# Kernel tuning notes

Measured on AMD Instinct MI355X. Metric: run time of the kernel, lower is better.

## Reference

```python
import jax, jax.numpy as jnp
import numpy as np
import math

N_HEADS = 8

def _head_dirs():
    # 8 trigrams = corners of {-1,+1}^3, L2-normalized -> each row / sqrt(3)
    t = np.array([[ (i >> 2 & 1) * 2 - 1, (i >> 1 & 1) * 2 - 1, (i & 1) * 2 - 1]
                  for i in range(8)], dtype=np.float32)
    return jnp.asarray(t / np.sqrt(3.0, dtype=np.float32))

def setup_inputs() -> dict:
    key = jax.random.key(0)
    k1, k2, k3, k4 = jax.random.split(key, 4)
    B, T, C = 2, 2048, 1024
    x = jax.random.normal(k1, (B, T, C), dtype=jnp.float32)
    w_qkv = jax.random.normal(k2, (C, 3 * C), dtype=jnp.float32) * (1.0 / math.sqrt(C))
    w_out = jax.random.normal(k3, (C, C), dtype=jnp.float32) * (1.0 / math.sqrt(C))
    head_scales = jax.random.normal(k4, (N_HEADS,), dtype=jnp.float32) * 0.1
    return {"x": x, "w_qkv": w_qkv, "w_out": w_out, "head_scales": head_scales}

def reference(x, w_qkv, w_out, head_scales):
    B, T, C = x.shape
    H = N_HEADS
    hd = C // H
    scale = 1.0 / math.sqrt(hd)
    dirs = _head_dirs()  # [H,3], fixed buffer

    qkv = (x @ w_qkv).reshape(B, T, 3, H, hd)
    q = jnp.transpose(qkv[:, :, 0], (0, 2, 1, 3))  # [B,H,T,hd]
    k = jnp.transpose(qkv[:, :, 1], (0, 2, 1, 3))
    v = jnp.transpose(qkv[:, :, 2], (0, 2, 1, 3))

    scores = jnp.einsum('bhqd,bhkd->bhqk', q, k) * scale  # [B,H,T,T]
    causal = jnp.tril(jnp.ones((T, T), dtype=bool))
    scores = jnp.where(causal[None, None], scores, -jnp.inf)

    # rank-1 geometric (trigram) bias on first 3 dims of q,k
    q_proj = jnp.einsum('bhtd,hd->bht', q[..., :3], dirs)  # [B,H,T]
    k_proj = jnp.einsum('bhtd,hd->bht', k[..., :3], dirs)
    geo = q_proj[..., :, None] * k_proj[..., None, :]       # [B,H,T,T]
    scores = scores + head_scales[None, :, None, None] * geo

    attn = jax.nn.softmax(scores, axis=-1)
    out = jnp.einsum('bhqk,bhkd->bqhd', attn, v).reshape(B, T, C)
    return out @ w_out
```

## Files before the change

### kernel.cpp

```cpp
#include <hip/hip_runtime.h>
#include <hip/hip_bf16.h>
#include <cstdint>
#include <cstddef>


namespace {
constexpr int kB = 2, kT = 2048, kC = 1024, kHD = 128;
constexpr int kM = kB * kT;
constexpr int kN3 = 3 * kC;
constexpr float kScale = 0.08838834764831845f;
constexpr float kInvS3 = 0.57735026918962576f;
constexpr float kL2E  = 1.4426950408889634f;
}

typedef __bf16 bf16x8 __attribute__((ext_vector_type(8)));
typedef float f32x4 __attribute__((ext_vector_type(4)));
typedef unsigned short u16x8 __attribute__((ext_vector_type(8)));
typedef unsigned short u16x4 __attribute__((ext_vector_type(4)));
typedef unsigned int u32x4 __attribute__((ext_vector_type(4)));

__device__ __forceinline__ unsigned short f2b(float f) {
  return __builtin_bit_cast(unsigned short, (__bf16)f);
}
__device__ __forceinline__ float b2f(unsigned short u) {
  return (float)__builtin_bit_cast(__bf16, u);
}
__device__ __forceinline__ void gll16(const void* g, void* lds) {
  __builtin_amdgcn_global_load_lds(
      (const __attribute__((address_space(1))) unsigned int*)g,
      (__attribute__((address_space(3))) unsigned int*)lds, 16, 0, 0);
}
__device__ __forceinline__ bf16x8 ldsv(const unsigned short* p) {
  return __builtin_bit_cast(bf16x8, *(const u16x8*)p);
}
__device__ __forceinline__ uint2 tr16(const unsigned short* p) {
  uint2 r;
  unsigned off = (unsigned)(uintptr_t)(const __attribute__((address_space(3))) unsigned short*)p;
  asm volatile("ds_read_b64_tr_b16 %0, %1" : "=v"(r) : "v"(off));
  return r;
}

__global__ void k_cvt(const float* __restrict__ in, unsigned short* __restrict__ out, int n4) {
  int i = blockIdx.x * 256 + threadIdx.x;
  if (i >= n4) return;
  float4 v = ((const float4*)in)[i];
  u16x4 o = { f2b(v.x), f2b(v.y), f2b(v.z), f2b(v.w) };
  ((u16x4*)out)[i] = o;
}

__global__ void k_tc(const float* __restrict__ in, unsigned short* __restrict__ out,
                     int R, int Cin) {
  __shared__ float tile[64][65];
  const int t = threadIdx.x;
  const int r0 = blockIdx.y * 64, c0 = blockIdx.x * 64;
  const int tr = t >> 4, tc4 = (t & 15) * 4;
#pragma unroll
  for (int rr = 0; rr < 4; ++rr) {
    int r = tr + rr * 16;
    float4 v = *(const float4*)&in[(size_t)(r0 + r) * Cin + c0 + tc4];
    tile[r][tc4 + 0] = v.x; tile[r][tc4 + 1] = v.y;
    tile[r][tc4 + 2] = v.z; tile[r][tc4 + 3] = v.w;
  }
  __syncthreads();
#pragma unroll
  for (int rr = 0; rr < 4; ++rr) {
    int c = tr + rr * 16;
    u16x4 o = { f2b(tile[tc4 + 0][c]), f2b(tile[tc4 + 1][c]),
                f2b(tile[tc4 + 2][c]), f2b(tile[tc4 + 3][c]) };
    *(u16x4*)&out[(size_t)(c0 + c) * R + r0 + tc4] = o;
  }
}

__global__ __launch_bounds__(256, 2) void k_gemm(
    const unsigned short* __restrict__ A,
    const unsigned short* __restrict__ Bt,
    unsigned short* __restrict__ Cb,
    float* __restrict__ Cf,
    int M, int N, int K, int ldc) {
  __shared__ unsigned short sA[2][4096];
  __shared__ unsigned short sB[2][4096];
  const int t = threadIdx.x;
  const int lane = t & 63, wave = t >> 6;
  const int g = lane >> 4, c16 = lane & 15;
  const int wr = wave >> 1, wc = wave & 1;
  const int brow = blockIdx.x * 128, bcol = blockIdx.y * 128;
  const int NT = K >> 5;

  f32x4 acc[4][4];
#pragma unroll
  for (int m = 0; m < 4; ++m)
#pragma unroll
    for (int n = 0; n < 4; ++n) acc[m][n] = 0.f;

  auto stage = [&](int buf, int kt) {
    const int k0 = kt * 32;
#pragma unroll
    for (int is = 0; is < 2; ++is) {
      int row = is * 64 + (t >> 2);
      int gs = (t & 3) ^ (row & 3);
      gll16(&A[(size_t)(brow + row) * K + k0 + gs * 8], &sA[buf][is * 2048 + wave * 512]);
      gll16(&Bt[(size_t)(bcol + row) * K + k0 + gs * 8], &sB[buf][is * 2048 + wave * 512]);
    }
  };

  stage(0, 0);
  __syncthreads();
  for (int kt = 0; kt < NT; ++kt) {
    if (kt + 1 < NT) stage((kt + 1) & 1, kt + 1);
    const int buf = kt & 1;
    bf16x8 av[4], bv[4];
#pragma unroll
    for (int m = 0; m < 4; ++m) {
      int row = wr * 64 + m * 16 + c16;
      av[m] = ldsv(&sA[buf][row * 32 + (g ^ (row & 3)) * 8]);
    }
#pragma unroll
    for (int n = 0; n < 4; ++n) {
      int row = wc * 64 + n * 16 + c16;
      bv[n] = ldsv(&sB[buf][row * 32 + (g ^ (row & 3)) * 8]);
    }
    __builtin_amdgcn_s_setprio(1);
#pragma unroll
    for (int m = 0; m < 4; ++m)
#pragma unroll
      for (int n = 0; n < 4; ++n)
        acc[m][n] = __builtin_amdgcn_mfma_f32_16x16x32_bf16(av[m], bv[n], acc[m][n], 0, 0, 0);
    __builtin_amdgcn_s_setprio(0);
    __syncthreads();
  }

  const int orow = brow + wr * 64, ocol = bcol + wc * 64;
  if (Cb != nullptr) {
#pragma unroll
    for (int m = 0; m < 4; ++m)
#pragma unroll
      for (int n = 0; n < 4; ++n)
#pragma unroll
        for (int jj = 0; jj < 4; ++jj)
          Cb[(size_t)(orow + m * 16 + g * 4 + jj) * ldc + ocol + n * 16 + c16] =
              f2b(acc[m][n][jj]);
  } else {
#pragma unroll
    for (int m = 0; m < 4; ++m)
#pragma unroll
      for (int n = 0; n < 4; ++n)
#pragma unroll
        for (int jj = 0; jj < 4; ++jj)
          Cf[(size_t)(orow + m * 16 + g * 4 + jj) * ldc + ocol + n * 16 + c16] =
              acc[m][n][jj];
  }
}

__global__ __launch_bounds__(512, 2) void k_gemm256(
    const unsigned short* __restrict__ A,
    const unsigned short* __restrict__ Bt,
    unsigned short* __restrict__ Cb,
    int M, int N, int K) {
  __shared__ unsigned short sA[2][16384];
  __shared__ unsigned short sB[2][16384];
  const int t = threadIdx.x;
  const int lane = t & 63, wave = t >> 6;
  const int gq = lane >> 4, c16 = lane & 15;
  const int wr = wave >> 2, wc = wave & 3;

  const int nbx = M >> 8;
  const int nwg = nbx * (N >> 8);
  const int bid = (int)blockIdx.x;
  const int swz = (bid & 7) * (nwg >> 3) + (bid >> 3);
  const int brow = (swz % nbx) * 256, bcol = (swz / nbx) * 256;
  const int NT = K >> 6;

  f32x4 acc[8][4];
#pragma unroll
  for (int m = 0; m < 8; ++m)
#pragma unroll
    for (int n = 0; n < 4; ++n) acc[m][n] = 0.f;

  auto stage = [&](int kt, int buf) {
    const int k0 = kt * 64;
#pragma unroll
    for (int j = 0; j < 4; ++j) {
      const int idx = j * 512 + t;
      const int row = idx >> 3, slot = idx & 7;
      const int ks = slot ^ (row & 7);
      const int dst = (j * 512 + wave * 64) * 8;
      gll16(&A[(size_t)(brow + row) * K + k0 + ks * 8], &sA[buf][dst]);
      gll16(&Bt[(size_t)(bcol + row) * K + k0 + ks * 8], &sB[buf][dst]);
    }
  };

  stage(0, 0);
  if (NT > 1) stage(1, 1);

  for (int kt = 0; kt < NT; ++kt) {
    const int buf = kt & 1;
    if (kt + 1 < NT) {
      asm volatile("s_waitcnt vmcnt(8)" ::: "memory");
    } else {
      asm volatile("s_waitcnt vmcnt(0)" ::: "memory");
    }
    __builtin_amdgcn_s_barrier();
    __builtin_amdgcn_sched_barrier(0);

#pragma unroll
    for (int ksub = 0; ksub < 2; ++ksub) {
      bf16x8 bv[4], av[8];
#pragma unroll
      for (int n = 0; n < 4; ++n) {
        int row = wc * 64 + n * 16 + c16;
        bv[n] = ldsv(&sB[buf][row * 64 + ((ksub * 4 + gq) ^ (row & 7)) * 8]);
      }
#pragma unroll
      for (int m = 0; m < 8; ++m) {
        int row = wr * 128 + m * 16 + c16;
        av[m] = ldsv(&sA[buf][row * 64 + ((ksub * 4 + gq) ^ (row & 7)) * 8]);
      }
      __builtin_amdgcn_s_setprio(1);
#pragma unroll
      for (int m = 0; m < 8; ++m)
#pragma unroll
        for (int n = 0; n < 4; ++n)
          acc[m][n] = __builtin_amdgcn_mfma_f32_16x16x32_bf16(av[m], bv[n], acc[m][n], 0, 0, 0);
      __builtin_amdgcn_s_setprio(0);
    }

    __builtin_amdgcn_s_barrier();
    if (kt + 2 < NT) stage(kt + 2, buf);
  }

  const int orow = brow + wr * 128, ocol = bcol + wc * 64;
#pragma unroll
  for (int m = 0; m < 8; ++m)
#pragma unroll
    for (int n = 0; n < 4; ++n)
#pragma unroll
      for (int jj = 0; jj < 4; ++jj)
        Cb[(size_t)(orow + m * 16 + gq * 4 + jj) * N + ocol + n * 16 + c16] =
            f2b(acc[m][n][jj]);
}

__constant__ unsigned char kItem[44] = {
  60, 61,
  62, 56, 57, 58, 52,
  53, 54, 48, 49,
  50, 44, 45, 46, 40,
  41, 42, 36, 37,
  38, 32, 33, 34, 28,
  29, 30, 24, 25,
  26, 20, 21, 22, 16,
  17, 18, 12, 13, 8, 9,
  14, 4, 5, 0 };

__global__ __launch_bounds__(256, 2) void k_attn(
    const unsigned short* __restrict__ qkv,
    const float* __restrict__ head_scales,
    unsigned short* __restrict__ pO0,
    unsigned short* __restrict__ pO1,
    unsigned short* __restrict__ pO2,
    float2* __restrict__ pml) {
  __shared__ unsigned short sK[8192];
  __shared__ unsigned short sV[2][8192];
  __shared__ float sKp[2][64];

  const int t = threadIdx.x;
  const int lane = t & 63, wave = t >> 6;
  const int g = lane >> 4, c16 = lane & 15;
  const int bh = blockIdx.x;
  const int it = kItem[blockIdx.y];
  const int qt = it >> 2, c = it & 3;
  const int n = 2 * qt + 2;
  const int nc = (qt == 0) ? 1 : (qt <= 2) ? 2 : 3;
  const int cbase = n / nc, crem = n % nc;
  const int t0 = c * cbase + (c < crem ? c : crem);
  const int t1 = t0 + cbase + (c < crem ? 1 : 0);

  const int b = bh >> 3, h = bh & 7;
  const float hs = head_scales[h];
  const float sx = (h & 4) ? 1.f : -1.f;
  const float sy = (h & 2) ? 1.f : -1.f;
  const float sz = (h & 1) ? 1.f : -1.f;

  const int q0w = qt * 128 + wave * 32;
  const size_t rowbase = (size_t)b * kT;

  bf16x8 aq[2][4];
  float qp[2];
#pragma unroll
  for (int m = 0; m < 2; ++m) {
    const unsigned short* qrow = &qkv[(rowbase + q0w + m * 16 + c16) * kN3 + h * kHD];
#pragma unroll
    for (int ks = 0; ks < 4; ++ks) aq[m][ks] = ldsv(qrow + ks * 32 + g * 8);
    qp[m] = hs * kInvS3 * (sx * b2f(qrow[0]) + sy * b2f(qrow[1]) + sz * b2f(qrow[2]));
  }

  float mrow[2] = { -__builtin_inff(), -__builtin_inff() };
  float lrow[2] = { 0.f, 0.f };
  f32x4 oacc[2][8];
#pragma unroll
  for (int m = 0; m < 2; ++m)
#pragma unroll
    for (int dn = 0; dn < 8; ++dn) oacc[m][dn] = 0.f;

  uint2 kpr;

  auto stageK = [&](int jt) {
    const int j0 = jt * 64;
#pragma unroll
    for (int is = 0; is < 4; ++is) {
      int row = is * 16 + (t >> 4);
      int gp = t & 15;
      int gs = (gp & 8) | ((gp ^ (row & 7)) & 7);
      gll16(&qkv[(rowbase + j0 + row) * kN3 + kC + h * kHD + gs * 8],
            &sK[is * 2048 + wave * 512]);
    }
  };
  auto stageV = [&](int jt, int buf) {
    const int j0 = jt * 64;
    const int vrow = ((lane >> 3) << 2) + ((lane >> 1) & 3);
    const int vcol = (lane & 1) * 8;
#pragma unroll
    for (int d = 0; d < 2; ++d) {
      const int dn = wave * 2 + d;
#pragma unroll
      for (int hf2 = 0; hf2 < 2; ++hf2) {
        gll16(&qkv[(rowbase + j0 + hf2 * 32 + vrow) * kN3 + 2 * kC + h * kHD
                   + dn * 16 + vcol],
              &sV[buf][dn * 1024 + hf2 * 512]);
      }
    }
  };
  auto loadKp = [&](int jt) {
    if (wave == 0)
      kpr = *(const uint2*)&qkv[(rowbase + jt * 64 + lane) * kN3 + kC + h * kHD];
  };
  auto writeKp = [&](int buf) {
    if (wave == 0) {
      float e0 = b2f((unsigned short)(kpr.x & 0xffffu));
      float e1 = b2f((unsigned short)(kpr.x >> 16));
      float e2 = b2f((unsigned short)(kpr.y & 0xffffu));
      sKp[buf][lane] = kInvS3 * (sx * e0 + sy * e1 + sz * e2);
    }
  };

  stageK(t0); stageV(t0, 0); loadKp(t0);
  writeKp(0);
  __syncthreads();

  for (int jt = t0; jt < t1; ++jt) {
    const int vbuf = (jt - t0) & 1;
    const bool more = (jt + 1 < t1);
    const int j0 = jt * 64;

    f32x4 s[2][4];
#pragma unroll
    for (int m = 0; m < 2; ++m)
#pragma unroll
      for (int nn = 0; nn < 4; ++nn) s[m][nn] = 0.f;
#pragma unroll
    for (int ks = 0; ks < 4; ++ks) {
      bf16x8 kb[4];
#pragma unroll
      for (int nn = 0; nn < 4; ++nn) {
        int gp = ks * 4 + g;
        int gp2 = (gp & 8) | ((gp ^ (c16 & 7)) & 7);
        kb[nn] = ldsv(&sK[(nn * 16 + c16) * 128 + gp2 * 8]);
      }
      __builtin_amdgcn_s_setprio(1);
#pragma unroll
      for (int m = 0; m < 2; ++m)
#pragma unroll
        for (int nn = 0; nn < 4; ++nn)
          s[m][nn] = __builtin_amdgcn_mfma_f32_16x16x32_bf16(kb[nn], aq[m][ks], s[m][nn], 0, 0, 0);
      __builtin_amdgcn_s_setprio(0);
    }

    __syncthreads();
    if (more) { stageK(jt + 1); stageV(jt + 1, vbuf ^ 1); loadKp(jt + 1); }

    float kpv[4][4];
#pragma unroll
    for (int nn = 0; nn < 4; ++nn)
#pragma unroll
      for (int jj = 0; jj < 4; ++jj) kpv[nn][jj] = sKp[vbuf][nn * 16 + g * 4 + jj];

    const bool edge = (jt >= 2 * qt);
    unsigned int paf[2][2][4];
#pragma unroll
    for (int m = 0; m < 2; ++m) {
      const int qg = q0w + m * 16 + c16;
      float vmax = -__builtin_inff();
#pragma unroll
      for (int nn = 0; nn < 4; ++nn)
#pragma unroll
        for (int jj = 0; jj < 4; ++jj) {
          float xv = s[m][nn][jj] * kScale + qp[m] * kpv[nn][jj];
          if (edge) {
            int kvg = j0 + nn * 16 + g * 4 + jj;
            xv = (kvg <= qg) ? xv : -__builtin_inff();
          }
          s[m][nn][jj] = xv;
          vmax = fmaxf(vmax, xv);
        }
      vmax = fmaxf(vmax, __shfl_xor(vmax, 16, 64));
      vmax = fmaxf(vmax, __shfl_xor(vmax, 32, 64));

      if (__any(vmax > mrow[m] + 8.f)) {
        float mnew = fmaxf(mrow[m], vmax);
        float mc0 = fmaxf(mnew, -1e30f);
        float alpha = exp2f((mrow[m] - mc0) * kL2E);
        mrow[m] = mnew;
        lrow[m] *= alpha;
        float ao[4];
#pragma unroll
        for (int jj = 0; jj < 4; ++jj)
          ao[jj] = __shfl(alpha, (lane & 48) | (g * 4 + jj), 64);
#pragma unroll
        for (int dn = 0; dn < 8; ++dn)
#pragma unroll
          for (int jj = 0; jj < 4; ++jj) oacc[m][dn][jj] *= ao[jj];
      }

      unsigned int pk[4][2];
      {
        const float mc = fmaxf(mrow[m], -1e30f);
        float ls = 0.f;
#pragma unroll
        for (int nn = 0; nn < 4; ++nn) {
          float p0 = exp2f((s[m][nn][0] - mc) * kL2E);
          float p1 = exp2f((s[m][nn][1] - mc) * kL2E);
          float p2 = exp2f((s[m][nn][2] - mc) * kL2E);
          float p3 = exp2f((s[m][nn][3] - mc) * kL2E);
          ls += (p0 + p1) + (p2 + p3);
          pk[nn][0] = (unsigned)f2b(p0) | ((unsigned)f2b(p1) << 16);
          pk[nn][1] = (unsigned)f2b(p2) | ((unsigned)f2b(p3) << 16);
        }
        lrow[m] += ls;
      }
#pragma unroll
      for (int ks2 = 0; ks2 < 2; ++ks2)
#pragma unroll
        for (int w = 0; w < 4; ++w) {
          int src = c16 + (((lane >> 4) & 1) * 2 + (w >> 1)) * 16;
          int va  = __shfl((int)pk[2 * ks2][w & 1], src, 64);
          int vb_ = __shfl((int)pk[2 * ks2 + 1][w & 1], src, 64);
          paf[m][ks2][w] = (unsigned)((lane & 32) ? vb_ : va);
        }
    }

#pragma unroll
    for (int ks2 = 0; ks2 < 2; ++ks2) {
      bf16x8 pa0 = __builtin_bit_cast(bf16x8,
          (u32x4){paf[0][ks2][0], paf[0][ks2][1], paf[0][ks2][2], paf[0][ks2][3]});
      bf16x8 pa1 = __builtin_bit_cast(bf16x8,
          (u32x4){paf[1][ks2][0], paf[1][ks2][1], paf[1][ks2][2], paf[1][ks2][3]});
      uint2 trv[8][2];
#pragma unroll
      for (int dn = 0; dn < 8; ++dn)
#pragma unroll
        for (int hf = 0; hf < 2; ++hf)
          trv[dn][hf] = tr16(&sV[vbuf][dn * 1024 + (ks2 * 8 + 2 * g + hf) * 64 + c16 * 4]);
      asm volatile("s_waitcnt lgkmcnt(0)" ::: "memory");
      __builtin_amdgcn_sched_barrier(0);
      __builtin_amdgcn_s_setprio(1);
#pragma unroll
      for (int dn = 0; dn < 8; ++dn) {
        bf16x8 vb = __builtin_bit_cast(bf16x8,
            (u32x4){trv[dn][0].x, trv[dn][0].y, trv[dn][1].x, trv[dn][1].y});
        oacc[0][dn] = __builtin_amdgcn_mfma_f32_16x16x32_bf16(pa0, vb, oacc[0][dn], 0, 0, 0);
        oacc[1][dn] = __builtin_amdgcn_mfma_f32_16x16x32_bf16(pa1, vb, oacc[1][dn], 0, 0, 0);
      }
      __builtin_amdgcn_s_setprio(0);
    }

    if (more) {
      writeKp(vbuf ^ 1);
      __syncthreads();
    }
  }

  unsigned short* pout = (c == 0) ? pO0 : (c == 1) ? pO1 : pO2;
#pragma unroll
  for (int m = 0; m < 2; ++m) {
    float lt = lrow[m];
    lt += __shfl_xor(lt, 16, 64);
    lt += __shfl_xor(lt, 32, 64);
    if (g == 0) {
      int rowi = wave * 32 + m * 16 + c16;
      pml[c * 32768 + (bh * 16 + qt) * 128 + rowi] = make_float2(mrow[m], lt);
    }
#pragma unroll
    for (int dn = 0; dn < 8; ++dn)
#pragma unroll
      for (int jj = 0; jj < 4; ++jj) {
        int r = q0w + m * 16 + g * 4 + jj;
        pout[(rowbase + r) * kC + h * kHD + dn * 16 + c16] = f2b(oacc[m][dn][jj]);
      }
  }
}

__global__ void k_comb(unsigned short* __restrict__ p0,
                       const unsigned short* __restrict__ p1,
                       const unsigned short* __restrict__ p2,
                       const float2* __restrict__ pml) {
  const int bh = blockIdx.x, qt = blockIdx.y;
  const int t = threadIdx.x;
  const int row = t >> 1, half = t & 1;
  const int b = bh >> 3, h = bh & 7;
  const size_t base = ((size_t)b * kT + qt * 128 + row) * kC + h * kHD + half * 64;
  const int nc = (qt == 0) ? 1 : (qt <= 2) ? 2 : 3;
  const int mli = (bh * 16 + qt) * 128 + row;
  float2 ml0 = pml[mli];
  float2 ml1 = make_float2(-1e30f, 0.f), ml2 = make_float2(-1e30f, 0.f);
  float mm = ml0.x;
  if (nc > 1) { ml1 = pml[32768 + mli]; mm = fmaxf(mm, ml1.x); }
  if (nc > 2) { ml2 = pml[65536 + mli]; mm = fmaxf(mm, ml2.x); }
  const float w0 = exp2f((ml0.x - mm) * kL2E);
  const float w1 = (nc > 1) ? exp2f((ml1.x - mm) * kL2E) : 0.f;
  const float w2 = (nc > 2) ? exp2f((ml2.x - mm) * kL2E) : 0.f;
  const float inv = 1.0f / (w0 * ml0.y + w1 * ml1.y + w2 * ml2.y);
#pragma unroll
  for (int i = 0; i < 8; ++i) {
    u16x8 o0 = *(const u16x8*)&p0[base + i * 8];
    u16x8 r;
    if (nc == 1) {
#pragma unroll
      for (int j = 0; j < 8; ++j) r[j] = f2b(b2f(o0[j]) * inv);
    } else if (nc == 2) {
      u16x8 o1 = *(const u16x8*)&p1[base + i * 8];
#pragma unroll
      for (int j = 0; j < 8; ++j)
        r[j] = f2b((w0 * b2f(o0[j]) + w1 * b2f(o1[j])) * inv);
    } else {
      u16x8 o1 = *(const u16x8*)&p1[base + i * 8];
      u16x8 o2 = *(const u16x8*)&p2[base + i * 8];
#pragma unroll
      for (int j = 0; j < 8; ++j)
        r[j] = f2b((w0 * b2f(o0[j]) + w1 * b2f(o1[j]) + w2 * b2f(o2[j])) * inv);
    }
    *(u16x8*)&p0[base + i * 8] = r;
  }
}

extern "C" void kernel_launch(void* const* d_in, const int* in_sizes, int n_in,
                              void* d_out, int out_size, void* d_ws, size_t ws_size,
                              hipStream_t stream) {
  const float* x    = (const float*)d_in[0];
  const float* wqkv = (const float*)d_in[1];
  const float* wout = (const float*)d_in[2];
  const float* hsc  = (const float*)d_in[3];
  char* ws = (char*)d_ws;
  unsigned short* xb    = (unsigned short*)(ws);
  unsigned short* wqkvT = (unsigned short*)(ws + 8388608);
  unsigned short* qkvb  = (unsigned short*)(ws + 16777216);
  unsigned short* attnb = (unsigned short*)(ws + 41943040);
  unsigned short* woutT = (unsigned short*)(ws);
  float2* pml = (float2*)d_out;
  float* out = (float*)d_out;

  k_cvt<<<dim3(4096), dim3(256), 0, stream>>>(x, xb, kM * kC / 4);
  k_tc<<<dim3(48, 16), dim3(256), 0, stream>>>(wqkv, wqkvT, kC, kN3);
  k_gemm256<<<dim3(192), dim3(512), 0, stream>>>(xb, wqkvT, qkvb, kM, kN3, kC);
  k_attn<<<dim3(16, 44), dim3(256), 0, stream>>>(qkvb, hsc, attnb, xb, wqkvT, pml);
  k_comb<<<dim3(16, 16), dim3(256), 0, stream>>>(attnb, xb, wqkvT, pml);
  k_tc<<<dim3(16, 16), dim3(256), 0, stream>>>(wout, woutT, kC, kC);
  k_gemm<<<dim3(32, 8), dim3(256), 0, stream>>>(attnb, woutT, nullptr, out, kM, kC, kC, kC);
}
```

Measured before the change: 138.3 us.

## Fuse prep and combine launches, interleave gemm256 prefetch with quarter-tile MFMA

Merges the x conversion and w_qkv transpose into one launch, and the partial-attention combine and w_out transpose into another, which removes two kernel launches. woutT moves to the qkv workspace region because xb and wqkvT are still read by the combine step. The 256x256 QKV GEMM changes from a two-stage prefetch to a single-tile-ahead scheme. Each quarter of the tile's MFMA work now issues one slice of the next tile's global-to-LDS loads. The cost is more barriers and a full vmcnt(0) wait every k-step, which may expose more memory latency.

```diff
diff --git a/kernel.cpp b/kernel.cpp
--- a/kernel.cpp
+++ b/kernel.cpp
@@ -40,19 +40,11 @@
   return r;
 }
 
-__global__ void k_cvt(const float* __restrict__ in, unsigned short* __restrict__ out, int n4) {
-  int i = blockIdx.x * 256 + threadIdx.x;
-  if (i >= n4) return;
-  float4 v = ((const float4*)in)[i];
-  u16x4 o = { f2b(v.x), f2b(v.y), f2b(v.z), f2b(v.w) };
-  ((u16x4*)out)[i] = o;
-}
-
-__global__ void k_tc(const float* __restrict__ in, unsigned short* __restrict__ out,
-                     int R, int Cin) {
+__device__ __forceinline__ void tc_body(const float* __restrict__ in,
+                                        unsigned short* __restrict__ out,
+                                        int R, int Cin, int bx, int by, int t) {
   __shared__ float tile[64][65];
-  const int t = threadIdx.x;
-  const int r0 = blockIdx.y * 64, c0 = blockIdx.x * 64;
+  const int r0 = by * 64, c0 = bx * 64;
   const int tr = t >> 4, tc4 = (t & 15) * 4;
 #pragma unroll
   for (int rr = 0; rr < 4; ++rr) {
@@ -68,6 +60,21 @@
     u16x4 o = { f2b(tile[tc4 + 0][c]), f2b(tile[tc4 + 1][c]),
                 f2b(tile[tc4 + 2][c]), f2b(tile[tc4 + 3][c]) };
     *(u16x4*)&out[(size_t)(c0 + c) * R + r0 + tc4] = o;
+  }
+}
+
+__global__ void k_prep(const float* __restrict__ x, unsigned short* __restrict__ xb,
+                       const float* __restrict__ wqkv, unsigned short* __restrict__ wqkvT) {
+  const int bid = (int)blockIdx.x;
+  const int t = threadIdx.x;
+  if (bid < 4096) {
+    int i = bid * 256 + t;
+    float4 v = ((const float4*)x)[i];
+    u16x4 o = { f2b(v.x), f2b(v.y), f2b(v.z), f2b(v.w) };
+    ((u16x4*)xb)[i] = o;
+  } else {
+    int r = bid - 4096;
+    tc_body(wqkv, wqkvT, kC, kN3, r % 48, r / 48, t);
   }
 }
 
@@ -176,56 +183,58 @@
 #pragma unroll
     for (int n = 0; n < 4; ++n) acc[m][n] = 0.f;
 
-  auto stage = [&](int kt, int buf) {
+  auto stage_part = [&](int kt, int buf, int j) {
     const int k0 = kt * 64;
-#pragma unroll
-    for (int j = 0; j < 4; ++j) {
-      const int idx = j * 512 + t;
-      const int row = idx >> 3, slot = idx & 7;
-      const int ks = slot ^ (row & 7);
-      const int dst = (j * 512 + wave * 64) * 8;
-      gll16(&A[(size_t)(brow + row) * K + k0 + ks * 8], &sA[buf][dst]);
-      gll16(&Bt[(size_t)(bcol + row) * K + k0 + ks * 8], &sB[buf][dst]);
-    }
+    const int idx = j * 512 + t;
+    const int row = idx >> 3, slot = idx & 7;
+    const int ks = slot ^ (row & 7);
+    const int dst = (j * 512 + wave * 64) * 8;
+    gll16(&A[(size_t)(brow + row) * K + k0 + ks * 8], &sA[buf][dst]);
+    gll16(&Bt[(size_t)(bcol + row) * K + k0 + ks * 8], &sB[buf][dst]);
   };
 
-  stage(0, 0);
-  if (NT > 1) stage(1, 1);
+#pragma unroll
+  for (int j = 0; j < 4; ++j) stage_part(0, 0, j);
 
   for (int kt = 0; kt < NT; ++kt) {
     const int buf = kt & 1;
-    if (kt + 1 < NT) {
-      asm volatile("s_waitcnt vmcnt(8)" ::: "memory");
-    } else {
-      asm volatile("s_waitcnt vmcnt(0)" ::: "memory");
-    }
+    const bool pre = (kt + 1 < NT);
+    asm volatile("s_waitcnt vmcnt(0)" ::: "memory");
     __builtin_amdgcn_s_barrier();
-    __builtin_amdgcn_sched_barrier(0);
-
-#pragma unroll
-    for (int ksub = 0; ksub < 2; ++ksub) {
-      bf16x8 bv[4], av[8];
-#pragma unroll
-      for (int n = 0; n < 4; ++n) {
-        int row = wc * 64 + n * 16 + c16;
-        bv[n] = ldsv(&sB[buf][row * 64 + ((ksub * 4 + gq) ^ (row & 7)) * 8]);
-      }
-#pragma unroll
-      for (int m = 0; m < 8; ++m) {
-        int row = wr * 128 + m * 16 + c16;
-        av[m] = ldsv(&sA[buf][row * 64 + ((ksub * 4 + gq) ^ (row & 7)) * 8]);
-      }
+
+#pragma unroll
+    for (int q = 0; q < 4; ++q) {
+      const int mh = q >> 1, nh = q & 1;
+      bf16x8 av[4][2], bv[2][2];
+#pragma unroll
+      for (int ksub = 0; ksub < 2; ++ksub) {
+#pragma unroll
+        for (int mf = 0; mf < 4; ++mf) {
+          int row = wr * 128 + mh * 64 + mf * 16 + c16;
+          av[mf][ksub] = ldsv(&sA[buf][row * 64 + ((ksub * 4 + gq) ^ (row & 7)) * 8]);
+        }
+#pragma unroll
+        for (int nf = 0; nf < 2; ++nf) {
+          int row = wc * 64 + nh * 32 + nf * 16 + c16;
+          bv[nf][ksub] = ldsv(&sB[buf][row * 64 + ((ksub * 4 + gq) ^ (row & 7)) * 8]);
+        }
+      }
+      if (pre) stage_part(kt + 1, buf ^ 1, q);
+      __builtin_amdgcn_s_barrier();
+      asm volatile("s_waitcnt lgkmcnt(0)" ::: "memory");
+      __builtin_amdgcn_sched_barrier(0);
       __builtin_amdgcn_s_setprio(1);
 #pragma unroll
-      for (int m = 0; m < 8; ++m)
-#pragma unroll
-        for (int n = 0; n < 4; ++n)
-          acc[m][n] = __builtin_amdgcn_mfma_f32_16x16x32_bf16(av[m], bv[n], acc[m][n], 0, 0, 0);
+      for (int ksub = 0; ksub < 2; ++ksub)
+#pragma unroll
+        for (int mf = 0; mf < 4; ++mf)
+#pragma unroll
+          for (int nf = 0; nf < 2; ++nf)
+            acc[mh * 4 + mf][nh * 2 + nf] = __builtin_amdgcn_mfma_f32_16x16x32_bf16(
+                av[mf][ksub], bv[nf][ksub], acc[mh * 4 + mf][nh * 2 + nf], 0, 0, 0);
       __builtin_amdgcn_s_setprio(0);
-    }
-
-    __builtin_amdgcn_s_barrier();
-    if (kt + 2 < NT) stage(kt + 2, buf);
+      __builtin_amdgcn_s_barrier();
+    }
   }
 
   const int orow = brow + wr * 128, ocol = bcol + wc * 64;
@@ -498,12 +507,20 @@
   }
 }
 
-__global__ void k_comb(unsigned short* __restrict__ p0,
-                       const unsigned short* __restrict__ p1,
-                       const unsigned short* __restrict__ p2,
-                       const float2* __restrict__ pml) {
-  const int bh = blockIdx.x, qt = blockIdx.y;
+__global__ void k_fin(unsigned short* __restrict__ p0,
+                      const unsigned short* __restrict__ p1,
+                      const unsigned short* __restrict__ p2,
+                      const float2* __restrict__ pml,
+                      const float* __restrict__ wout,
+                      unsigned short* __restrict__ woutT) {
+  const int bid = (int)blockIdx.x;
   const int t = threadIdx.x;
+  if (bid >= 256) {
+    int r = bid - 256;
+    tc_body(wout, woutT, kC, kC, r & 15, r >> 4, t);
+    return;
+  }
+  const int bh = bid & 15, qt = bid >> 4;
   const int row = t >> 1, half = t & 1;
   const int b = bh >> 3, h = bh & 7;
   const size_t base = ((size_t)b * kT + qt * 128 + row) * kC + h * kHD + half * 64;
@@ -553,15 +570,13 @@
   unsigned short* wqkvT = (unsigned short*)(ws + 8388608);
   unsigned short* qkvb  = (unsigned short*)(ws + 16777216);
   unsigned short* attnb = (unsigned short*)(ws + 41943040);
-  unsigned short* woutT = (unsigned short*)(ws);
+  unsigned short* woutT = (unsigned short*)(ws + 16777216);
   float2* pml = (float2*)d_out;
   float* out = (float*)d_out;
 
-  k_cvt<<<dim3(4096), dim3(256), 0, stream>>>(x, xb, kM * kC / 4);
-  k_tc<<<dim3(48, 16), dim3(256), 0, stream>>>(wqkv, wqkvT, kC, kN3);
+  k_prep<<<dim3(4864), dim3(256), 0, stream>>>(x, xb, wqkv, wqkvT);
   k_gemm256<<<dim3(192), dim3(512), 0, stream>>>(xb, wqkvT, qkvb, kM, kN3, kC);
   k_attn<<<dim3(16, 44), dim3(256), 0, stream>>>(qkvb, hsc, attnb, xb, wqkvT, pml);
-  k_comb<<<dim3(16, 16), dim3(256), 0, stream>>>(attnb, xb, wqkvT, pml);
-  k_tc<<<dim3(16, 16), dim3(256), 0, stream>>>(wout, woutT, kC, kC);
+  k_fin<<<dim3(512), dim3(256), 0, stream>>>(attnb, xb, wqkvT, pml, wout, woutT);
   k_gemm<<<dim3(32, 8), dim3(256), 0, stream>>>(attnb, woutT, nullptr, out, kM, kC, kC, kC);
 }
```

New measurement: 136.0 us. Within noise of the previous version (-1.7%).
